# Kernel tuning notes

Hardware: AMD Instinct MI355X
Metric: run time of the kernel (lower is better)

The kernel has to match this reference:

```python
import jax, jax.numpy as jnp
import numpy as np

# kernel / loss hyperparameters (from base_params)
FIT_SIGMA = 1.0
FIT_L = 1.0
MMD_SIGMA = 1.0
MMD_L = 2.0
REG_LAMBDA = 0.01

N, D = 8192, 16


def setup_inputs() -> dict:
    key = jax.random.key(0)
    k1, k2, k3 = jax.random.split(key, 3)
    X = jax.random.normal(k1, (N, D), dtype=jnp.float32)
    Y = jax.random.normal(k2, (N, D), dtype=jnp.float32)
    Lam = jax.random.normal(k3, (N, D), dtype=jnp.float32)  # nn.init.normal_ on zeros(N,d)
    return {"X": X, "Y": Y, "Lam": Lam}


def _rbf_gram(X, sigma, l):
    # k(xi, xj) = sigma^2 * exp(-||xi - xj||^2 / (2 l^2)), vectorized over all pairs
    sq = jnp.sum(X * X, axis=1)                      # [N]
    d2 = sq[:, None] + sq[None, :] - 2.0 * (X @ X.T)  # [N, N] squared distances
    d2 = jnp.maximum(d2, 0.0)
    return (sigma ** 2) * jnp.exp(-d2 / (2.0 * l ** 2))


def reference(X, Y, Lam):
    fit_kXX = _rbf_gram(X, FIT_SIGMA, FIT_L)   # [N, N]
    mmd_kXX = _rbf_gram(X, MMD_SIGMA, MMD_L)   # [N, N]
    diff = fit_kXX @ Lam - Y                   # [N, d]
    # trace(diff^T K diff) = sum(diff * (K @ diff))
    loss_fit = jnp.sum(diff * (mmd_kXX @ diff))
    loss_reg = REG_LAMBDA * jnp.sum(Lam * (fit_kXX @ Lam))
    return loss_fit + loss_reg
```

## Files before the change

### kernel.cpp

```cpp
#include <hip/hip_runtime.h>

#define NPTS 8192
#define DIM  16

constexpr int BLK = 256;
constexpr int NIB = NPTS / BLK;

#define REG_LAMBDA 0.01f

typedef _Float16 h8 __attribute__((ext_vector_type(8)));
typedef float    f4 __attribute__((ext_vector_type(4)));

__device__ __forceinline__ float dot4(float4 a, float4 b) {
  return fmaf(a.x, b.x, fmaf(a.y, b.y, fmaf(a.z, b.z, a.w * b.w)));
}
__device__ __forceinline__ void add4(float4& a, float4 b) {
  a.x += b.x; a.y += b.y; a.z += b.z; a.w += b.w;
}

__device__ __forceinline__ float block_sum(float v, float* wbuf) {
#pragma unroll
  for (int o = 32; o > 0; o >>= 1) v += __shfl_down(v, o, 64);
  const int lane = threadIdx.x & 63;
  const int wid  = threadIdx.x >> 6;
  __syncthreads();
  if (lane == 0) wbuf[wid] = v;
  __syncthreads();
  float s = 0.f;
  if (threadIdx.x == 0) {
#pragma unroll
    for (int w = 0; w < BLK / 64; ++w) s += wbuf[w];
  }
  return s;
}

__global__ __launch_bounds__(BLK) void k_prep(
    const float4* __restrict__ Xv, const float4* __restrict__ Lv,
    _Float16* __restrict__ Xh, _Float16* __restrict__ LamT,
    float* __restrict__ csq1, float* __restrict__ csq2) {
  const int i = blockIdx.x * BLK + threadIdx.x;
  float sqsum = 0.f;
  _Float16* xr = Xh + (size_t)i * DIM;
#pragma unroll
  for (int q = 0; q < 4; ++q) {
    const float4 v = Xv[(size_t)i * 4 + q];
    const _Float16 h0 = (_Float16)v.x, h1 = (_Float16)v.y;
    const _Float16 h2 = (_Float16)v.z, h3 = (_Float16)v.w;
    xr[4 * q + 0] = h0; xr[4 * q + 1] = h1;
    xr[4 * q + 2] = h2; xr[4 * q + 3] = h3;
    const float f0 = (float)h0, f1 = (float)h1, f2 = (float)h2, f3 = (float)h3;
    sqsum += f0 * f0 + f1 * f1 + f2 * f2 + f3 * f3;
    const float4 l = Lv[(size_t)i * 4 + q];
    LamT[(size_t)(4 * q + 0) * NPTS + i] = (_Float16)l.x;
    LamT[(size_t)(4 * q + 1) * NPTS + i] = (_Float16)l.y;
    LamT[(size_t)(4 * q + 2) * NPTS + i] = (_Float16)l.z;
    LamT[(size_t)(4 * q + 3) * NPTS + i] = (_Float16)l.w;
  }
  csq1[i] = -0.5f   * sqsum;
  csq2[i] = -0.125f * sqsum;
}

__global__ __launch_bounds__(BLK) void k_pass1(
    const _Float16* __restrict__ Xh, const _Float16* __restrict__ LamT,
    const float* __restrict__ csq1, float* __restrict__ Upart, int span) {
  __shared__ __align__(16) _Float16 sP[4][16][32];
  const int lane = threadIdx.x & 63;
  const int w    = threadIdx.x >> 6;
  const int l16  = lane & 15;
  const int quad = lane >> 4;
  const h8 hz = (h8)(_Float16)0.f;

  ((h8*)&sP[w][0][0])[lane] = hz;

  const int i0 = blockIdx.x * 64 + w * 16;
  h8 ax = hz;
  if (quad < 2) ax = *(const h8*)(Xh + (size_t)(i0 + l16) * DIM + quad * 8);
  const int ir = i0 + quad * 4;
  f4 ci;
  ci[0] = csq1[ir + 0]; ci[1] = csq1[ir + 1];
  ci[2] = csq1[ir + 2]; ci[3] = csq1[ir + 3];

  f4 U = (f4)0.f;
  const int jbeg = blockIdx.y * span;
  const int jend = jbeg + span;
#pragma unroll 2
  for (int j0 = jbeg; j0 < jend; j0 += 16) {
    h8 bx = hz;
    if (quad < 2) bx = *(const h8*)(Xh + (size_t)(j0 + l16) * DIM + quad * 8);
    const float cj = csq1[j0 + l16];
    const f4 dot = __builtin_amdgcn_mfma_f32_16x16x32_f16(ax, bx, (f4)0.f, 0, 0, 0);
#pragma unroll
    for (int r = 0; r < 4; ++r) {
      const float p = __expf(dot[r] + ci[r] + cj);
      sP[w][quad * 4 + r][l16] = (_Float16)p;
    }
    const h8 ap = *(const h8*)&sP[w][l16][quad * 8];
    const h8 bl = *(const h8*)(LamT + (size_t)l16 * NPTS + j0 + quad * 8);
    U = __builtin_amdgcn_mfma_f32_16x16x32_f16(ap, bl, U, 0, 0, 0);
  }

  float* dst = Upart + ((size_t)blockIdx.y * NPTS + i0) * DIM;
#pragma unroll
  for (int r = 0; r < 4; ++r)
    dst[(quad * 4 + r) * DIM + l16] = U[r];
}

__global__ __launch_bounds__(BLK) void k_reduce(
    const float4* __restrict__ Upart, const float4* __restrict__ Yv,
    const float4* __restrict__ Lv, _Float16* __restrict__ Dh,
    float* __restrict__ accums, int jc) {
  __shared__ float wred[BLK / 64];
  const int i = blockIdx.x * BLK + threadIdx.x;
  float4 u0 = {0.f, 0.f, 0.f, 0.f}, u1 = u0, u2 = u0, u3 = u0;
  for (int c = 0; c < jc; ++c) {
    const float4* p = Upart + ((size_t)c * NPTS + i) * 4;
    add4(u0, p[0]); add4(u1, p[1]); add4(u2, p[2]); add4(u3, p[3]);
  }
  const float4 y0 = Yv[(size_t)i * 4 + 0];
  const float4 y1 = Yv[(size_t)i * 4 + 1];
  const float4 y2 = Yv[(size_t)i * 4 + 2];
  const float4 y3 = Yv[(size_t)i * 4 + 3];
  _Float16* dr = Dh + (size_t)i * DIM;
  dr[0]  = (_Float16)(u0.x - y0.x); dr[1]  = (_Float16)(u0.y - y0.y);
  dr[2]  = (_Float16)(u0.z - y0.z); dr[3]  = (_Float16)(u0.w - y0.w);
  dr[4]  = (_Float16)(u1.x - y1.x); dr[5]  = (_Float16)(u1.y - y1.y);
  dr[6]  = (_Float16)(u1.z - y1.z); dr[7]  = (_Float16)(u1.w - y1.w);
  dr[8]  = (_Float16)(u2.x - y2.x); dr[9]  = (_Float16)(u2.y - y2.y);
  dr[10] = (_Float16)(u2.z - y2.z); dr[11] = (_Float16)(u2.w - y2.w);
  dr[12] = (_Float16)(u3.x - y3.x); dr[13] = (_Float16)(u3.y - y3.y);
  dr[14] = (_Float16)(u3.z - y3.z); dr[15] = (_Float16)(u3.w - y3.w);

  const float4 l0 = Lv[(size_t)i * 4 + 0];
  const float4 l1 = Lv[(size_t)i * 4 + 1];
  const float4 l2 = Lv[(size_t)i * 4 + 2];
  const float4 l3 = Lv[(size_t)i * 4 + 3];
  const float regp = (dot4(l0, u0) + dot4(l1, u1)) + (dot4(l2, u2) + dot4(l3, u3));
  const float rtot = block_sum(regp, wred);
  if (threadIdx.x == 0) unsafeAtomicAdd(&accums[1], rtot);
}

__global__ __launch_bounds__(BLK) void k_pass2(
    const _Float16* __restrict__ Xh, const _Float16* __restrict__ Dh,
    const float* __restrict__ csq2, float* __restrict__ accums, int span) {
  __shared__ float wred[BLK / 64];
  const int lane = threadIdx.x & 63;
  const int w    = threadIdx.x >> 6;
  const int l16  = lane & 15;
  const int quad = lane >> 4;
  const h8 hz = (h8)(_Float16)0.f;

  const int i0 = blockIdx.x * 128 + w * 32;
  h8 ax0 = hz, ax1 = hz, ad0 = hz, ad1 = hz;
  if (quad < 2) {
    ax0 = *(const h8*)(Xh + (size_t)(i0 + l16) * DIM + quad * 8);
    ax1 = *(const h8*)(Xh + (size_t)(i0 + 16 + l16) * DIM + quad * 8);
    ad0 = *(const h8*)(Dh + (size_t)(i0 + l16) * DIM + quad * 8);
    ad1 = *(const h8*)(Dh + (size_t)(i0 + 16 + l16) * DIM + quad * 8);
  }
  const int ir = i0 + quad * 4;
  f4 ci0, ci1;
#pragma unroll
  for (int r = 0; r < 4; ++r) { ci0[r] = csq2[ir + r]; ci1[r] = csq2[ir + 16 + r]; }

  float s = 0.f;
  const int jbeg = blockIdx.y * span;
  const int jend = jbeg + span;
  for (int j0 = jbeg; j0 < jend; j0 += 16) {
    h8 bx = hz, bd = hz;
    if (quad < 2) {
      bx = *(const h8*)(Xh + (size_t)(j0 + l16) * DIM + quad * 8);
      bd = *(const h8*)(Dh + (size_t)(j0 + l16) * DIM + quad * 8);
    }
    const float cj = csq2[j0 + l16];
    const f4 dx0 = __builtin_amdgcn_mfma_f32_16x16x32_f16(ax0, bx, (f4)0.f, 0, 0, 0);
    const f4 dd0 = __builtin_amdgcn_mfma_f32_16x16x32_f16(ad0, bd, (f4)0.f, 0, 0, 0);
    const f4 dx1 = __builtin_amdgcn_mfma_f32_16x16x32_f16(ax1, bx, (f4)0.f, 0, 0, 0);
    const f4 dd1 = __builtin_amdgcn_mfma_f32_16x16x32_f16(ad1, bd, (f4)0.f, 0, 0, 0);
#pragma unroll
    for (int r = 0; r < 4; ++r) {
      s = fmaf(__expf(fmaf(0.25f, dx0[r], ci0[r] + cj)), dd0[r], s);
      s = fmaf(__expf(fmaf(0.25f, dx1[r], ci1[r] + cj)), dd1[r], s);
    }
  }

  const float stot = block_sum(s, wred);
  if (threadIdx.x == 0) unsafeAtomicAdd(&accums[0], stot);
}

__global__ void k_final(const float* __restrict__ accums, float* __restrict__ out) {
  out[0] = accums[0] + REG_LAMBDA * accums[1];
}

extern "C" void kernel_launch(void* const* d_in, const int* in_sizes, int n_in,
                              void* d_out, int out_size, void* d_ws, size_t ws_size,
                              hipStream_t stream) {
  const float4* Xv = (const float4*)d_in[0];
  const float4* Yv = (const float4*)d_in[1];
  const float4* Lv = (const float4*)d_in[2];
  float* out = (float*)d_out;

  char* base = (char*)d_ws;
  _Float16* Xh   = (_Float16*)(base);
  _Float16* LamT = (_Float16*)(base + 256 * 1024);
  _Float16* Dh   = (_Float16*)(base + 512 * 1024);
  float*    csq1 = (float*)(base + 768 * 1024);
  float*    csq2 = (float*)(base + 800 * 1024);
  float*    accums = (float*)(base + 832 * 1024);
  float*    Upart  = (float*)(base + 832 * 1024 + 256);
  const size_t fixed = 832 * 1024 + 256;

  int jc = 8;
  while (jc > 1 && fixed + (size_t)jc * NPTS * DIM * 4 > ws_size) jc >>= 1;
  const int span1 = NPTS / jc;
  const int jc2 = 16, span2 = NPTS / jc2;

  hipMemsetAsync(accums, 0, 2 * sizeof(float), stream);
  k_prep<<<NIB, BLK, 0, stream>>>(Xv, Lv, Xh, LamT, csq1, csq2);
  k_pass1<<<dim3(NPTS / 64, jc), BLK, 0, stream>>>(Xh, LamT, csq1, Upart, span1);
  k_reduce<<<NIB, BLK, 0, stream>>>((const float4*)Upart, Yv, Lv, Dh, accums, jc);
  k_pass2<<<dim3(NPTS / 128, jc2), BLK, 0, stream>>>(Xh, Dh, csq2, accums, span2);
  k_final<<<1, 1, 0, stream>>>(accums, out);
}
```

Measured before the change: 135.3 us.

## Use 16x16x16 MFMA with prescaled X, exp2, and register-resident P tiles

```diff
diff --git a/kernel.cpp b/kernel.cpp
--- a/kernel.cpp
+++ b/kernel.cpp
@@ -7,9 +7,19 @@
 constexpr int NIB = NPTS / BLK;
 
 #define REG_LAMBDA 0.01f
-
-typedef _Float16 h8 __attribute__((ext_vector_type(8)));
+#define C1 1.2011224087864498f
+#define C2 0.6005612043932249f
+
+typedef _Float16 h4 __attribute__((ext_vector_type(4)));
 typedef float    f4 __attribute__((ext_vector_type(4)));
+
+#define MFMA16(a, b, c) __builtin_amdgcn_mfma_f32_16x16x16f16((a), (b), (c), 0, 0, 0)
+
+#if __has_builtin(__builtin_amdgcn_exp2f)
+#define EXP2(x) __builtin_amdgcn_exp2f(x)
+#else
+#define EXP2(x) exp2f(x)
+#endif
 
 __device__ __forceinline__ float dot4(float4 a, float4 b) {
   return fmaf(a.x, b.x, fmaf(a.y, b.y, fmaf(a.z, b.z, a.w * b.w)));
@@ -36,73 +46,80 @@
 
 __global__ __launch_bounds__(BLK) void k_prep(
     const float4* __restrict__ Xv, const float4* __restrict__ Lv,
-    _Float16* __restrict__ Xh, _Float16* __restrict__ LamT,
+    _Float16* __restrict__ Xh1, _Float16* __restrict__ Xh2,
+    _Float16* __restrict__ LamT,
     float* __restrict__ csq1, float* __restrict__ csq2) {
   const int i = blockIdx.x * BLK + threadIdx.x;
-  float sqsum = 0.f;
-  _Float16* xr = Xh + (size_t)i * DIM;
+  float sq1 = 0.f, sq2 = 0.f;
+  h4* x1 = (h4*)(Xh1 + (size_t)i * DIM);
+  h4* x2 = (h4*)(Xh2 + (size_t)i * DIM);
 #pragma unroll
   for (int q = 0; q < 4; ++q) {
     const float4 v = Xv[(size_t)i * 4 + q];
-    const _Float16 h0 = (_Float16)v.x, h1 = (_Float16)v.y;
-    const _Float16 h2 = (_Float16)v.z, h3 = (_Float16)v.w;
-    xr[4 * q + 0] = h0; xr[4 * q + 1] = h1;
-    xr[4 * q + 2] = h2; xr[4 * q + 3] = h3;
-    const float f0 = (float)h0, f1 = (float)h1, f2 = (float)h2, f3 = (float)h3;
-    sqsum += f0 * f0 + f1 * f1 + f2 * f2 + f3 * f3;
+    h4 a = {(_Float16)(C1 * v.x), (_Float16)(C1 * v.y),
+            (_Float16)(C1 * v.z), (_Float16)(C1 * v.w)};
+    h4 b = {(_Float16)(C2 * v.x), (_Float16)(C2 * v.y),
+            (_Float16)(C2 * v.z), (_Float16)(C2 * v.w)};
+    x1[q] = a; x2[q] = b;
+#pragma unroll
+    for (int t = 0; t < 4; ++t) {
+      const float fa = (float)a[t], fb = (float)b[t];
+      sq1 = fmaf(fa, fa, sq1);
+      sq2 = fmaf(fb, fb, sq2);
+    }
     const float4 l = Lv[(size_t)i * 4 + q];
     LamT[(size_t)(4 * q + 0) * NPTS + i] = (_Float16)l.x;
     LamT[(size_t)(4 * q + 1) * NPTS + i] = (_Float16)l.y;
     LamT[(size_t)(4 * q + 2) * NPTS + i] = (_Float16)l.z;
     LamT[(size_t)(4 * q + 3) * NPTS + i] = (_Float16)l.w;
   }
-  csq1[i] = -0.5f   * sqsum;
-  csq2[i] = -0.125f * sqsum;
+  csq1[i] = -0.5f * sq1;
+  csq2[i] = -0.5f * sq2;
 }
 
 __global__ __launch_bounds__(BLK) void k_pass1(
-    const _Float16* __restrict__ Xh, const _Float16* __restrict__ LamT,
+    const _Float16* __restrict__ Xh1, const _Float16* __restrict__ LamT,
     const float* __restrict__ csq1, float* __restrict__ Upart, int span) {
-  __shared__ __align__(16) _Float16 sP[4][16][32];
   const int lane = threadIdx.x & 63;
   const int w    = threadIdx.x >> 6;
   const int l16  = lane & 15;
   const int quad = lane >> 4;
-  const h8 hz = (h8)(_Float16)0.f;
-
-  ((h8*)&sP[w][0][0])[lane] = hz;
-
-  const int i0 = blockIdx.x * 64 + w * 16;
-  h8 ax = hz;
-  if (quad < 2) ax = *(const h8*)(Xh + (size_t)(i0 + l16) * DIM + quad * 8);
-  const int ir = i0 + quad * 4;
-  f4 ci;
-  ci[0] = csq1[ir + 0]; ci[1] = csq1[ir + 1];
-  ci[2] = csq1[ir + 2]; ci[3] = csq1[ir + 3];
-
-  f4 U = (f4)0.f;
+
+  const int i0 = blockIdx.x * 128 + w * 32;
+  const h4 bxi0 = *(const h4*)(Xh1 + (size_t)(i0 + l16) * DIM + quad * 4);
+  const h4 bxi1 = *(const h4*)(Xh1 + (size_t)(i0 + 16 + l16) * DIM + quad * 4);
+  const float ci0 = csq1[i0 + l16];
+  const float ci1 = csq1[i0 + 16 + l16];
+  const _Float16* blrow = LamT + (size_t)l16 * NPTS;
+
+  f4 U0 = {0.f, 0.f, 0.f, 0.f}, U1 = U0;
   const int jbeg = blockIdx.y * span;
   const int jend = jbeg + span;
 #pragma unroll 2
   for (int j0 = jbeg; j0 < jend; j0 += 16) {
-    h8 bx = hz;
-    if (quad < 2) bx = *(const h8*)(Xh + (size_t)(j0 + l16) * DIM + quad * 8);
-    const float cj = csq1[j0 + l16];
-    const f4 dot = __builtin_amdgcn_mfma_f32_16x16x32_f16(ax, bx, (f4)0.f, 0, 0, 0);
+    const h4 axj = *(const h4*)(Xh1 + (size_t)(j0 + l16) * DIM + quad * 4);
+    const float4 cjf = *(const float4*)(csq1 + j0 + quad * 4);
+    const f4 cc0 = {cjf.x + ci0, cjf.y + ci0, cjf.z + ci0, cjf.w + ci0};
+    const f4 cc1 = {cjf.x + ci1, cjf.y + ci1, cjf.z + ci1, cjf.w + ci1};
+    const f4 p0 = MFMA16(axj, bxi0, cc0);
+    const f4 p1 = MFMA16(axj, bxi1, cc1);
+    h4 ap0, ap1;
 #pragma unroll
     for (int r = 0; r < 4; ++r) {
-      const float p = __expf(dot[r] + ci[r] + cj);
-      sP[w][quad * 4 + r][l16] = (_Float16)p;
+      ap0[r] = (_Float16)EXP2(p0[r]);
+      ap1[r] = (_Float16)EXP2(p1[r]);
     }
-    const h8 ap = *(const h8*)&sP[w][l16][quad * 8];
-    const h8 bl = *(const h8*)(LamT + (size_t)l16 * NPTS + j0 + quad * 8);
-    U = __builtin_amdgcn_mfma_f32_16x16x32_f16(ap, bl, U, 0, 0, 0);
+    const h4 bl = *(const h4*)(blrow + j0 + quad * 4);
+    U0 = MFMA16(ap0, bl, U0);
+    U1 = MFMA16(ap1, bl, U1);
   }
 
   float* dst = Upart + ((size_t)blockIdx.y * NPTS + i0) * DIM;
 #pragma unroll
-  for (int r = 0; r < 4; ++r)
-    dst[(quad * 4 + r) * DIM + l16] = U[r];
+  for (int r = 0; r < 4; ++r) {
+    dst[(quad * 4 + r) * DIM + l16]        = U0[r];
+    dst[(16 + quad * 4 + r) * DIM + l16]   = U1[r];
+  }
 }
 
 __global__ __launch_bounds__(BLK) void k_reduce(
@@ -110,76 +127,56 @@
     const float4* __restrict__ Lv, _Float16* __restrict__ Dh,
     float* __restrict__ accums, int jc) {
   __shared__ float wred[BLK / 64];
-  const int i = blockIdx.x * BLK + threadIdx.x;
-  float4 u0 = {0.f, 0.f, 0.f, 0.f}, u1 = u0, u2 = u0, u3 = u0;
-  for (int c = 0; c < jc; ++c) {
-    const float4* p = Upart + ((size_t)c * NPTS + i) * 4;
-    add4(u0, p[0]); add4(u1, p[1]); add4(u2, p[2]); add4(u3, p[3]);
-  }
-  const float4 y0 = Yv[(size_t)i * 4 + 0];
-  const float4 y1 = Yv[(size_t)i * 4 + 1];
-  const float4 y2 = Yv[(size_t)i * 4 + 2];
-  const float4 y3 = Yv[(size_t)i * 4 + 3];
-  _Float16* dr = Dh + (size_t)i * DIM;
-  dr[0]  = (_Float16)(u0.x - y0.x); dr[1]  = (_Float16)(u0.y - y0.y);
-  dr[2]  = (_Float16)(u0.z - y0.z); dr[3]  = (_Float16)(u0.w - y0.w);
-  dr[4]  = (_Float16)(u1.x - y1.x); dr[5]  = (_Float16)(u1.y - y1.y);
-  dr[6]  = (_Float16)(u1.z - y1.z); dr[7]  = (_Float16)(u1.w - y1.w);
-  dr[8]  = (_Float16)(u2.x - y2.x); dr[9]  = (_Float16)(u2.y - y2.y);
-  dr[10] = (_Float16)(u2.z - y2.z); dr[11] = (_Float16)(u2.w - y2.w);
-  dr[12] = (_Float16)(u3.x - y3.x); dr[13] = (_Float16)(u3.y - y3.y);
-  dr[14] = (_Float16)(u3.z - y3.z); dr[15] = (_Float16)(u3.w - y3.w);
-
-  const float4 l0 = Lv[(size_t)i * 4 + 0];
-  const float4 l1 = Lv[(size_t)i * 4 + 1];
-  const float4 l2 = Lv[(size_t)i * 4 + 2];
-  const float4 l3 = Lv[(size_t)i * 4 + 3];
-  const float regp = (dot4(l0, u0) + dot4(l1, u1)) + (dot4(l2, u2) + dot4(l3, u3));
+  const int t = blockIdx.x * BLK + threadIdx.x;
+  const int i = t >> 2, q = t & 3;
+  float4 u = {0.f, 0.f, 0.f, 0.f};
+  for (int c = 0; c < jc; ++c)
+    add4(u, Upart[((size_t)c * NPTS + i) * 4 + q]);
+  const float4 y = Yv[(size_t)i * 4 + q];
+  h4 d = {(_Float16)(u.x - y.x), (_Float16)(u.y - y.y),
+          (_Float16)(u.z - y.z), (_Float16)(u.w - y.w)};
+  *(h4*)(Dh + (size_t)i * DIM + q * 4) = d;
+  const float regp = dot4(Lv[(size_t)i * 4 + q], u);
   const float rtot = block_sum(regp, wred);
   if (threadIdx.x == 0) unsafeAtomicAdd(&accums[1], rtot);
 }
 
 __global__ __launch_bounds__(BLK) void k_pass2(
-    const _Float16* __restrict__ Xh, const _Float16* __restrict__ Dh,
+    const _Float16* __restrict__ Xh2, const _Float16* __restrict__ Dh,
     const float* __restrict__ csq2, float* __restrict__ accums, int span) {
   __shared__ float wred[BLK / 64];
   const int lane = threadIdx.x & 63;
   const int w    = threadIdx.x >> 6;
   const int l16  = lane & 15;
   const int quad = lane >> 4;
-  const h8 hz = (h8)(_Float16)0.f;
+  const f4 fz = {0.f, 0.f, 0.f, 0.f};
 
   const int i0 = blockIdx.x * 128 + w * 32;
-  h8 ax0 = hz, ax1 = hz, ad0 = hz, ad1 = hz;
-  if (quad < 2) {
-    ax0 = *(const h8*)(Xh + (size_t)(i0 + l16) * DIM + quad * 8);
-    ax1 = *(const h8*)(Xh + (size_t)(i0 + 16 + l16) * DIM + quad * 8);
-    ad0 = *(const h8*)(Dh + (size_t)(i0 + l16) * DIM + quad * 8);
-    ad1 = *(const h8*)(Dh + (size_t)(i0 + 16 + l16) * DIM + quad * 8);
-  }
-  const int ir = i0 + quad * 4;
-  f4 ci0, ci1;
-#pragma unroll
-  for (int r = 0; r < 4; ++r) { ci0[r] = csq2[ir + r]; ci1[r] = csq2[ir + 16 + r]; }
+  const h4 ax0 = *(const h4*)(Xh2 + (size_t)(i0 + l16) * DIM + quad * 4);
+  const h4 ax1 = *(const h4*)(Xh2 + (size_t)(i0 + 16 + l16) * DIM + quad * 4);
+  const h4 ad0 = *(const h4*)(Dh  + (size_t)(i0 + l16) * DIM + quad * 4);
+  const h4 ad1 = *(const h4*)(Dh  + (size_t)(i0 + 16 + l16) * DIM + quad * 4);
+  const float4 cif0 = *(const float4*)(csq2 + i0 + quad * 4);
+  const float4 cif1 = *(const float4*)(csq2 + i0 + 16 + quad * 4);
 
   float s = 0.f;
   const int jbeg = blockIdx.y * span;
   const int jend = jbeg + span;
+#pragma unroll 2
   for (int j0 = jbeg; j0 < jend; j0 += 16) {
-    h8 bx = hz, bd = hz;
-    if (quad < 2) {
-      bx = *(const h8*)(Xh + (size_t)(j0 + l16) * DIM + quad * 8);
-      bd = *(const h8*)(Dh + (size_t)(j0 + l16) * DIM + quad * 8);
-    }
+    const h4 bx = *(const h4*)(Xh2 + (size_t)(j0 + l16) * DIM + quad * 4);
+    const h4 bd = *(const h4*)(Dh  + (size_t)(j0 + l16) * DIM + quad * 4);
     const float cj = csq2[j0 + l16];
-    const f4 dx0 = __builtin_amdgcn_mfma_f32_16x16x32_f16(ax0, bx, (f4)0.f, 0, 0, 0);
-    const f4 dd0 = __builtin_amdgcn_mfma_f32_16x16x32_f16(ad0, bd, (f4)0.f, 0, 0, 0);
-    const f4 dx1 = __builtin_amdgcn_mfma_f32_16x16x32_f16(ax1, bx, (f4)0.f, 0, 0, 0);
-    const f4 dd1 = __builtin_amdgcn_mfma_f32_16x16x32_f16(ad1, bd, (f4)0.f, 0, 0, 0);
+    const f4 cc0 = {cif0.x + cj, cif0.y + cj, cif0.z + cj, cif0.w + cj};
+    const f4 cc1 = {cif1.x + cj, cif1.y + cj, cif1.z + cj, cif1.w + cj};
+    const f4 dx0 = MFMA16(ax0, bx, cc0);
+    const f4 dd0 = MFMA16(ad0, bd, fz);
+    const f4 dx1 = MFMA16(ax1, bx, cc1);
+    const f4 dd1 = MFMA16(ad1, bd, fz);
 #pragma unroll
     for (int r = 0; r < 4; ++r) {
-      s = fmaf(__expf(fmaf(0.25f, dx0[r], ci0[r] + cj)), dd0[r], s);
-      s = fmaf(__expf(fmaf(0.25f, dx1[r], ci1[r] + cj)), dd1[r], s);
+      s = fmaf(EXP2(dx0[r]), dd0[r], s);
+      s = fmaf(EXP2(dx1[r]), dd1[r], s);
     }
   }
 
@@ -200,24 +197,25 @@
   float* out = (float*)d_out;
 
   char* base = (char*)d_ws;
-  _Float16* Xh   = (_Float16*)(base);
-  _Float16* LamT = (_Float16*)(base + 256 * 1024);
-  _Float16* Dh   = (_Float16*)(base + 512 * 1024);
-  float*    csq1 = (float*)(base + 768 * 1024);
-  float*    csq2 = (float*)(base + 800 * 1024);
-  float*    accums = (float*)(base + 832 * 1024);
-  float*    Upart  = (float*)(base + 832 * 1024 + 256);
-  const size_t fixed = 832 * 1024 + 256;
-
-  int jc = 8;
+  _Float16* Xh1  = (_Float16*)(base);
+  _Float16* Xh2  = (_Float16*)(base + 256 * 1024);
+  _Float16* LamT = (_Float16*)(base + 512 * 1024);
+  _Float16* Dh   = (_Float16*)(base + 768 * 1024);
+  float*    csq1 = (float*)(base + 1024 * 1024);
+  float*    csq2 = (float*)(base + 1056 * 1024);
+  float*    accums = (float*)(base + 1088 * 1024);
+  float*    Upart  = (float*)(base + 1088 * 1024 + 256);
+  const size_t fixed = 1088 * 1024 + 256;
+
+  int jc = 16;
   while (jc > 1 && fixed + (size_t)jc * NPTS * DIM * 4 > ws_size) jc >>= 1;
   const int span1 = NPTS / jc;
   const int jc2 = 16, span2 = NPTS / jc2;
 
   hipMemsetAsync(accums, 0, 2 * sizeof(float), stream);
-  k_prep<<<NIB, BLK, 0, stream>>>(Xv, Lv, Xh, LamT, csq1, csq2);
-  k_pass1<<<dim3(NPTS / 64, jc), BLK, 0, stream>>>(Xh, LamT, csq1, Upart, span1);
-  k_reduce<<<NIB, BLK, 0, stream>>>((const float4*)Upart, Yv, Lv, Dh, accums, jc);
-  k_pass2<<<dim3(NPTS / 128, jc2), BLK, 0, stream>>>(Xh, Dh, csq2, accums, span2);
+  k_prep<<<NIB, BLK, 0, stream>>>(Xv, Lv, Xh1, Xh2, LamT, csq1, csq2);
+  k_pass1<<<dim3(NPTS / 128, jc), BLK, 0, stream>>>(Xh1, LamT, csq1, Upart, span1);
+  k_reduce<<<NPTS * 4 / BLK, BLK, 0, stream>>>((const float4*)Upart, Yv, Lv, Dh, accums, jc);
+  k_pass2<<<dim3(NPTS / 128, jc2), BLK, 0, stream>>>(Xh2, Dh, csq2, accums, span2);
   k_final<<<1, 1, 0, stream>>>(accums, out);
 }
```

Result: faster. 120.6 us (-10.9%).
